# Kernel tuning notes

Measured on AMD Instinct MI355X. Metric: run time of the kernel, lower is better.

The kernel has to match this reference:

```python
import jax, jax.numpy as jnp
import numpy as np

EPS = 1e-5
NB, NP, NA, NROT = 16, 1024, 12, 60
C0, C1 = 64, 128
CIN, CFEAT, COUT = 256, 512, 256


def _bn(x, g, b):
    # training-mode BatchNorm1d: stats over batch (+ spatial) dims, channel dim 1
    axes = (0,) if x.ndim == 2 else (0, 2)
    m = x.mean(axis=axes, keepdims=True)
    v = x.var(axis=axes, keepdims=True)
    sh = [1] * x.ndim; sh[1] = -1
    return (x - m) * jax.lax.rsqrt(v + EPS) * g.reshape(sh) + b.reshape(sh)


def _hat(v):  # (n,3) -> (n,3,3) skew-symmetric
    z = jnp.zeros_like(v[:, 0])
    return jnp.stack([z, -v[:, 2], v[:, 1],
                      v[:, 2], z, -v[:, 0],
                      -v[:, 1], v[:, 0], z], axis=-1).reshape(-1, 3, 3)


def _exp_so3(v):  # Rodrigues formula, (n,3) -> (n,3,3)
    theta = jnp.linalg.norm(v, axis=-1, keepdims=True)  # (n,1)
    k = v / jnp.where(theta < 1e-8, 1.0, theta)
    K = _hat(k)
    s = jnp.sin(theta)[..., None]
    c = (1.0 - jnp.cos(theta))[..., None]
    I = jnp.eye(3, dtype=v.dtype)
    return I + s * K + c * (K @ K)


def _pointnet(xyz, feats, W, b, g, bb):
    # PointnetSO3Conv: concat xyz (expanded over anchors) with feats, 1x1 conv, max over points
    nb, _, npts, na = feats.shape
    x = jnp.concatenate([jnp.broadcast_to(xyz[:, :, :, None], (nb, 3, npts, na)), feats], axis=1)
    y = jnp.einsum('oc,bcpa->bopa', W, x) + b[None, :, None, None]
    y = y.max(axis=2)  # max over points -> (nb, o, na)
    return jax.nn.relu(_bn(y, g, bb))


def setup_inputs() -> dict:
    key = jax.random.key(0)
    ks = iter(jax.random.split(key, 64))
    def nrm(shape, s=0.1):
        return jax.random.normal(next(ks), shape, dtype=jnp.float32) * s
    d = {
        'xyz0': nrm((NB, 3, NP), 1.0),
        'feats0': nrm((NB, C0, NP, NA), 1.0),
        'xyz1': nrm((NB, 3, NP), 1.0),
        'feats1': nrm((NB, C1, NP, NA), 1.0),
        'trace_idx': jax.random.randint(next(ks), (NA, NROT), 0, NA),
        'anchors': nrm((NROT, 3, 3), 1.0),
        'pn0_W': nrm((C0, C0 + 3)), 'pn0_b': nrm((C0,)), 'pn0_g': jnp.ones((C0,), jnp.float32), 'pn0_bb': jnp.zeros((C0,), jnp.float32),
        'pn1_W': nrm((C1, C1 + 3)), 'pn1_b': nrm((C1,)), 'pn1_g': jnp.ones((C1,), jnp.float32), 'pn1_bb': jnp.zeros((C1,), jnp.float32),
        'lin_W': nrm((CIN, C0 + C1)), 'lin_b': nrm((CIN,)), 'lin_g': jnp.ones((CIN,), jnp.float32), 'lin_bb': jnp.zeros((CIN,), jnp.float32),
        'feat_W': nrm((CFEAT, CIN * NA)), 'feat_b': nrm((CFEAT,)), 'feat_g': jnp.ones((CFEAT,), jnp.float32), 'feat_bb': jnp.zeros((CFEAT,), jnp.float32),
        'att_W1': nrm((128, CFEAT)), 'att_b1': nrm((128,)), 'att_g': jnp.ones((128,), jnp.float32), 'att_bb': jnp.zeros((128,), jnp.float32),
        'att_W2': nrm((1, 128)), 'att_b2': nrm((1,)),
        'reg_W1': nrm((128, CFEAT)), 'reg_b1': nrm((128,)), 'reg_g': jnp.ones((128,), jnp.float32), 'reg_bb': jnp.zeros((128,), jnp.float32),
        'reg_W2': nrm((7, 128)), 'reg_b2': nrm((7,)),
        'out_W1': nrm((CFEAT, CFEAT)), 'out_b1': nrm((CFEAT,)), 'out_g': jnp.ones((CFEAT,), jnp.float32), 'out_bb': jnp.zeros((CFEAT,), jnp.float32),
        'out_W2': nrm((COUT, CFEAT)), 'out_b2': nrm((COUT,)),
    }
    return d


def reference(xyz0, feats0, xyz1, feats1, trace_idx, anchors,
              pn0_W, pn0_b, pn0_g, pn0_bb, pn1_W, pn1_b, pn1_g, pn1_bb,
              lin_W, lin_b, lin_g, lin_bb, feat_W, feat_b, feat_g, feat_bb,
              att_W1, att_b1, att_g, att_bb, att_W2, att_b2,
              reg_W1, reg_b1, reg_g, reg_bb, reg_W2, reg_b2,
              out_W1, out_b1, out_g, out_bb, out_W2, out_b2):
    nb = feats0.shape[0]
    # _pooling: per-level pointnet + BN + relu, concat, pn_linear + pn_bn
    p0 = _pointnet(xyz0, feats0, pn0_W, pn0_b, pn0_g, pn0_bb)
    p1 = _pointnet(xyz1, feats1, pn1_W, pn1_b, pn1_g, pn1_bb)
    x = jnp.concatenate([p0, p1], axis=1)                                   # (nb, 192, na)
    x = _bn(jnp.einsum('oc,bca->boa', lin_W, x) + lin_b[None, :, None], lin_g, lin_bb)  # (nb,256,na)
    # gather trace_idx_ori and flatten channel x anchor dims
    x = x[:, :, trace_idx].reshape(nb, CIN * NA, NROT)                      # (nb,3072,60)
    xf = jax.nn.relu(_bn(jnp.einsum('oc,bca->boa', feat_W, x) + feat_b[None, :, None], feat_g, feat_bb))  # (nb,512,60)
    h = jax.nn.relu(_bn(jnp.einsum('oc,bca->boa', reg_W1, xf) + reg_b1[None, :, None], reg_g, reg_bb))
    residual = (jnp.einsum('oc,bca->boa', reg_W2, h) + reg_b2[None, :, None]).transpose(0, 2, 1)  # (nb,60,7)
    res_D = residual[:, :, :3] / jnp.linalg.norm(residual[:, :, :3], axis=-1, keepdims=True)
    res_N = (jax.nn.sigmoid(residual[:, :, 3]) - 0.5) * jnp.pi / 5
    res_V = res_D * res_N[..., None]
    res_R = _exp_so3(res_V.reshape(-1, 3)).reshape(nb, NROT, 3, 3)
    res_T = residual[:, :, 4:]
    pred_R = jnp.einsum('tij,btjk->btik', anchors, res_R)
    # attention head + softmax over 60 rotations
    a = jax.nn.relu(_bn(jnp.einsum('oc,bca->boa', att_W1, xf) + att_b1[None, :, None], att_g, att_bb))
    logits = (jnp.einsum('oc,bca->boa', att_W2, a) + att_b2[None, :, None])[:, 0]   # (nb,60)
    x_attn = jax.nn.softmax(logits, axis=-1)
    # max-pool over rotations + out MLP
    xm = xf.max(axis=-1)                                                    # (nb,512)
    o = jax.nn.relu(_bn(xm @ out_W1.T + out_b1, out_g, out_bb))
    x_out = o @ out_W2.T + out_b2
    return (x_out, x_attn, pred_R, res_T)
```

## Files before the change

kernel.cpp:

```cpp
#include <hip/hip_runtime.h>
#include <math.h>

#define NBATCH 16
#define NPTS   1024
#define NANG   12
#define NROTS  60
#define EPSV   1e-5f

#define WB0_OFF   0
#define WB1_OFF   3072
#define PART0_OFF 13312
#define PART1_OFF 799744
#define XF_OFF    13312
#define XM_OFF    504832
#define OACT_OFF  513024
#define XCAT_OFF  2372608
#define XLIN_OFF  2409472
#define XG_OFF    2458624
#define BRP_OFF   2458624
#define HACT_OFF  4424704
#define AACT_OFF  4547584
#define FRAW_OFF  5407744
#define FEATW_OFF 6882304

#define OUT_XOUT 0
#define OUT_ATTN 4096
#define OUT_PRED 5056
#define OUT_REST 13696

typedef short  bf16x8 __attribute__((ext_vector_type(8)));
typedef float  f32x4  __attribute__((ext_vector_type(4)));

__device__ __forceinline__ unsigned short f2bf_rne(float x){
  unsigned int u = __float_as_uint(x);
  u += 0x7FFFu + ((u >> 16) & 1u);
  return (unsigned short)(u >> 16);
}
__device__ __forceinline__ float bf2f(unsigned short h){
  return __uint_as_float(((unsigned int)h) << 16);
}

__device__ __forceinline__ bf16x8 pack8(const float* f){
  union { unsigned int u[4]; bf16x8 v; } r;
  #pragma unroll
  for (int i = 0; i < 4; i++)
    r.u[i] = __builtin_amdgcn_perm(__float_as_uint(f[2*i+1]),
                                   __float_as_uint(f[2*i]), 0x07060302u);
  return r.v;
}

__device__ __forceinline__ void stage16(const unsigned short* g, unsigned short* l){
  __builtin_amdgcn_global_load_lds((const __attribute__((address_space(1))) void*)g,
                                   (__attribute__((address_space(3))) void*)l, 16, 0, 0);
}

template<int NT>
__device__ __forceinline__ void block_stats(float v, float& m, float& var, float* sbuf){
  constexpr int NW = NT / 64;
  float s = v, s2 = v * v;
  #pragma unroll
  for (int off = 32; off; off >>= 1){
    s  += __shfl_xor(s,  off, 64);
    s2 += __shfl_xor(s2, off, 64);
  }
  const int w = threadIdx.x >> 6;
  if ((threadIdx.x & 63) == 0){ sbuf[w] = s; sbuf[NW + w] = s2; }
  __syncthreads();
  float ts = 0.f, ts2 = 0.f;
  #pragma unroll
  for (int i = 0; i < NW; i++){ ts += sbuf[i]; ts2 += sbuf[NW + i]; }
  m = ts / (float)NT;
  var = ts2 / (float)NT - m * m;
}

template<int C>
__device__ __forceinline__ void prep_wb_body(int idx, const float* __restrict__ W,
                                             unsigned short* __restrict__ Wb){
  constexpr int KPAD = C + 32;
  if (idx >= C * KPAD) return;
  const int o = idx / KPAD, k = idx % KPAD;
  float v = 0.f;
  if (k < C)          v = W[(size_t)o * (C + 3) + 3 + k];
  else if (k < C + 3) v = W[(size_t)o * (C + 3) + (k - C)];
  Wb[idx] = f2bf_rne(v);
}

__global__ __launch_bounds__(256) void prep_all(
    const float* __restrict__ W0, const float* __restrict__ W1,
    const float* __restrict__ FW,
    unsigned short* __restrict__ wb0, unsigned short* __restrict__ wb1,
    unsigned short* __restrict__ fw2){
  const int blk = blockIdx.x;
  if (blk < 24){
    prep_wb_body<64>(blk * 256 + threadIdx.x, W0, wb0);
  } else if (blk < 104){
    prep_wb_body<128>((blk - 24) * 256 + threadIdx.x, W1, wb1);
  } else {
    const int idx = (blk - 104) * 256 + threadIdx.x;
    const int o = idx / 3072, k = idx % 3072;
    const float x = FW[idx];
    const unsigned short hi = f2bf_rne(x);
    const unsigned short lo = f2bf_rne(x - bf2f(hi));
    fw2[(size_t)o * 6144 + k] = hi;
    fw2[(size_t)o * 6144 + 3072 + k] = lo;
  }
}

#define SROW 196
template<int C>
__device__ __forceinline__ void pn_body(
    int nchunk, int b,
    const float* __restrict__ xyz, const float* __restrict__ feats,
    const unsigned short* __restrict__ Wb, float* __restrict__ part,
    float* yb ){
  constexpr int KPAD = C + 32;
  constexpr int NFK  = C / 32;
  constexpr int MTH  = C / 32;
  const int tid  = threadIdx.x;
  const int lane = tid & 63, w = tid >> 6;
  const int wo = w >> 2, wn = w & 3;
  const int g = lane >> 4, l16 = lane & 15;
  const int o_off = wo * (C / 2);
  const int nbase = nchunk * 192;

  int nn[3], pp[3];
  #pragma unroll
  for (int t = 0; t < 3; t++){
    nn[t] = wn * 48 + t * 16 + l16;
    pp[t] = (nbase + nn[t]) / 12;
  }

  f32x4 acc[MTH][3];
  #pragma unroll
  for (int m = 0; m < MTH; m++)
    #pragma unroll
    for (int t = 0; t < 3; t++)
      acc[m][t] = (f32x4){0.f, 0.f, 0.f, 0.f};

  const float* fB = feats + (size_t)b * C * (NPTS * NANG) + nbase;

  float fbuf[2][3][8];
  #pragma unroll
  for (int t = 0; t < 3; t++)
    #pragma unroll
    for (int j = 0; j < 8; j++)
      fbuf[0][t][j] = fB[(size_t)(g * 8 + j) * (NPTS * NANG) + nn[t]];

  #pragma unroll
  for (int ks = 0; ks < NFK; ks++){
    const int cur = ks & 1;
    if (ks + 1 < NFK){
      const int kb = (ks + 1) * 32;
      #pragma unroll
      for (int t = 0; t < 3; t++)
        #pragma unroll
        for (int j = 0; j < 8; j++)
          fbuf[cur ^ 1][t][j] = fB[(size_t)(kb + g * 8 + j) * (NPTS * NANG) + nn[t]];
    }
    const int kb = ks * 32;
    bf16x8 Bf[3];
    #pragma unroll
    for (int t = 0; t < 3; t++) Bf[t] = pack8(fbuf[cur][t]);
    #pragma unroll
    for (int m = 0; m < MTH; m++){
      const bf16x8 Af = *(const bf16x8*)(Wb + (size_t)(o_off + m * 16 + l16) * KPAD + kb + g * 8);
      #pragma unroll
      for (int t = 0; t < 3; t++)
        acc[m][t] = __builtin_amdgcn_mfma_f32_16x16x32_bf16(Af, Bf[t], acc[m][t], 0, 0, 0);
    }
  }

  {
    const int kb = C;
    bf16x8 Bf[3];
    #pragma unroll
    for (int t = 0; t < 3; t++){
      float f[8];
      #pragma unroll
      for (int j = 0; j < 8; j++) f[j] = 0.f;
      if (g == 0){
        #pragma unroll
        for (int j = 0; j < 3; j++)
          f[j] = xyz[(size_t)(b * 3 + j) * NPTS + pp[t]];
      }
      Bf[t] = pack8(f);
    }
    #pragma unroll
    for (int m = 0; m < MTH; m++){
      const bf16x8 Af = *(const bf16x8*)(Wb + (size_t)(o_off + m * 16 + l16) * KPAD + kb + g * 8);
      #pragma unroll
      for (int t = 0; t < 3; t++)
        acc[m][t] = __builtin_amdgcn_mfma_f32_16x16x32_bf16(Af, Bf[t], acc[m][t], 0, 0, 0);
    }
  }

  float* myb = yb + wo * (16 * SROW);
  #pragma unroll
  for (int m = 0; m < MTH; m++){
    __syncthreads();
    #pragma unroll
    for (int t = 0; t < 3; t++)
      #pragma unroll
      for (int r = 0; r < 4; r++)
        myb[(g * 4 + r) * SROW + nn[t]] = acc[m][t][r];
    __syncthreads();
    const int lt = tid & 255;
    if (lt < 192){
      const int o_l = lt / 12, a = lt % 12;
      float mx = -3.4e38f;
      #pragma unroll
      for (int pl = 0; pl < 16; pl++)
        mx = fmaxf(mx, myb[o_l * SROW + pl * 12 + a]);
      part[((size_t)(b * 64 + nchunk) * C + o_off + m * 16 + o_l) * 12 + a] = mx;
    }
  }
}

__global__ __launch_bounds__(512, 4) void pn_both(
    const float* __restrict__ xyz0, const float* __restrict__ feats0,
    const unsigned short* __restrict__ wb0, float* __restrict__ part0,
    const float* __restrict__ xyz1, const float* __restrict__ feats1,
    const unsigned short* __restrict__ wb1, float* __restrict__ part1){
  __shared__ float yb[2 * 16 * SROW];
  const int lin   = blockIdx.x + 64 * (blockIdx.y + 16 * blockIdx.z);
  const int which = lin & 1;
  const int rest  = lin >> 1;
  const int nchunk = rest & 63, b = rest >> 6;
  if (which == 0) pn_body<64> (nchunk, b, xyz0, feats0, wb0, part0, yb);
  else            pn_body<128>(nchunk, b, xyz1, feats1, wb1, part1, yb);
}

__global__ void pn_reduce_bn(const float* __restrict__ part0, const float* __restrict__ part1,
    const float* __restrict__ b0, const float* __restrict__ g0, const float* __restrict__ bb0,
    const float* __restrict__ b1, const float* __restrict__ g1, const float* __restrict__ bb1,
    float* __restrict__ xcat){
  const int ch = blockIdx.x, t = threadIdx.x;
  const int b = t / 12, a = t % 12;
  const float* part; const float *bias, *g, *bb; int o, Cl;
  if (ch < 64){ part = part0; bias = b0; g = g0; bb = bb0; o = ch;      Cl = 64;  }
  else        { part = part1; bias = b1; g = g1; bb = bb1; o = ch - 64; Cl = 128; }
  const float* pp = part + ((size_t)(b * 64) * Cl + o) * 12 + a;
  const size_t kstride = (size_t)Cl * 12;
  float v = pp[0];
  for (int k = 1; k < 64; k++) v = fmaxf(v, pp[(size_t)k * kstride]);
  v += bias[o];
  __shared__ float sbuf[8];
  float m, var;
  block_stats<192>(v, m, var, sbuf);
  float xn = (v - m) * rsqrtf(var + EPSV) * g[o] + bb[o];
  xcat[((size_t)b * 192 + ch) * 12 + a] = fmaxf(xn, 0.f);
}

__global__ void lin_bn(const float* __restrict__ xcat, const float* __restrict__ W,
    const float* __restrict__ bias, const float* __restrict__ g, const float* __restrict__ bb,
    float* __restrict__ xlin){
  const int o = blockIdx.x, t = threadIdx.x;
  const int b = t / 12, a = t % 12;
  const float* xr = xcat + (size_t)b * 2304 + a;
  const float* wr = W + (size_t)o * 192;
  float v = bias[o];
  for (int c = 0; c < 192; c++) v = fmaf(wr[c], xr[(size_t)c * 12], v);
  __shared__ float sbuf[8];
  float m, var;
  block_stats<192>(v, m, var, sbuf);
  xlin[((size_t)b * 256 + o) * 12 + a] = (v - m) * rsqrtf(var + EPSV) * g[o] + bb[o];
}

__global__ void prep_xg(const float* __restrict__ xlin, const int* __restrict__ trace,
                        unsigned short* __restrict__ Xg){
  const int n = blockIdx.x;
  const int b = n / 60, r = n % 60;
  unsigned short* row = Xg + (size_t)n * 6144;
  __shared__ int ta[12];
  if (threadIdx.x < 12) ta[threadIdx.x] = trace[threadIdx.x * 60 + r];
  __syncthreads();
  for (int i = threadIdx.x; i < 3072; i += 256){
    const int c = i / 12, a = i % 12;
    const float x = xlin[((size_t)b * 256 + c) * 12 + ta[a]];
    const unsigned short hi = f2bf_rne(x);
    const unsigned short lo = f2bf_rne(x - bf2f(hi));
    row[i] = hi;
    row[3072 + i] = lo;
  }
}

__global__ __launch_bounds__(256) void feat_mfma(
    const unsigned short* __restrict__ Wb2, const unsigned short* __restrict__ Xg,
    float* __restrict__ fraw){
  const int nblk = blockIdx.x, mblk = blockIdx.y, seg = blockIdx.z;
  const int tid = threadIdx.x;
  const int lane = tid & 63, wave = tid >> 6;
  const int g = lane >> 4, l16 = lane & 15;
  const int kA = (seg == 1) ? 3072 : 0;
  const int kB = (seg == 2) ? 3072 : 0;
  const int sw = l16 & 7;
  const int wm = wave >> 1, wn = wave & 1;

  __shared__ unsigned short As[2][64 * 64];
  __shared__ unsigned short Bs[2][64 * 64];

  int rowj[2], colj[2], ldsoff[2];
  #pragma unroll
  for (int j = 0; j < 2; j++){
    const int idx = j * 256 + wave * 64 + lane;
    rowj[j]   = idx >> 3;
    colj[j]   = ((idx & 7) ^ (rowj[j] & 7)) * 8;
    ldsoff[j] = (j * 256 + wave * 64) * 8;
  }
  const unsigned short* Agb = Wb2 + (size_t)mblk * 64 * 6144 + kA;
  const unsigned short* Bgb = Xg  + (size_t)nblk * 64 * 6144 + kB;

  f32x4 acc[2][2];
  #pragma unroll
  for (int i = 0; i < 2; i++)
    #pragma unroll
    for (int j = 0; j < 2; j++)
      acc[i][j] = (f32x4){0.f, 0.f, 0.f, 0.f};

  #pragma unroll
  for (int j = 0; j < 2; j++){
    stage16(Agb + (size_t)rowj[j] * 6144 + colj[j], &As[0][ldsoff[j]]);
    stage16(Bgb + (size_t)rowj[j] * 6144 + colj[j], &Bs[0][ldsoff[j]]);
  }
  __syncthreads();

  for (int kc = 0; kc < 3072; kc += 64){
    const int buf = (kc >> 6) & 1;
    if (kc + 64 < 3072){
      const int kn = kc + 64;
      #pragma unroll
      for (int j = 0; j < 2; j++){
        stage16(Agb + (size_t)rowj[j] * 6144 + kn + colj[j], &As[buf ^ 1][ldsoff[j]]);
        stage16(Bgb + (size_t)rowj[j] * 6144 + kn + colj[j], &Bs[buf ^ 1][ldsoff[j]]);
      }
    }
    #pragma unroll
    for (int kc2 = 0; kc2 < 64; kc2 += 32){
      const int c0 = kc2 >> 3;
      bf16x8 af[2], bfr[2];
      #pragma unroll
      for (int i = 0; i < 2; i++)
        af[i]  = *(const bf16x8*)&As[buf][(wm * 32 + i * 16 + l16) * 64 + ((c0 + g) ^ sw) * 8];
      #pragma unroll
      for (int i = 0; i < 2; i++)
        bfr[i] = *(const bf16x8*)&Bs[buf][(wn * 32 + i * 16 + l16) * 64 + ((c0 + g) ^ sw) * 8];
      #pragma unroll
      for (int i = 0; i < 2; i++)
        #pragma unroll
        for (int j = 0; j < 2; j++)
          acc[i][j] = __builtin_amdgcn_mfma_f32_16x16x32_bf16(af[i], bfr[j], acc[i][j], 0, 0, 0);
    }
    __syncthreads();
  }

  float* base = fraw + (size_t)seg * (512 * 960);
  #pragma unroll
  for (int i = 0; i < 2; i++)
    #pragma unroll
    for (int j = 0; j < 2; j++){
      const int n = nblk * 64 + wn * 32 + j * 16 + l16;
      #pragma unroll
      for (int q = 0; q < 4; q++){
        const int m = mblk * 64 + wm * 32 + i * 16 + g * 4 + q;
        base[(size_t)m * 960 + n] = acc[i][j][q];
      }
    }
}

__global__ void feat_bn(const float* __restrict__ fraw, const float* __restrict__ bias,
    const float* __restrict__ g, const float* __restrict__ bb,
    float* __restrict__ xf, float* __restrict__ xm){
  const int o = blockIdx.x, t = threadIdx.x;
  const int b = t / 60, r = t % 60;
  const size_t SS = (size_t)512 * 960;
  const size_t in = (size_t)o * 960 + t;
  float v = fraw[in] + fraw[SS + in] + fraw[2 * SS + in] + bias[o];
  __shared__ float sbuf[32];
  float m, var;
  block_stats<960>(v, m, var, sbuf);
  const float xn = fmaxf((v - m) * rsqrtf(var + EPSV) * g[o] + bb[o], 0.f);
  xf[((size_t)b * 512 + o) * 60 + r] = xn;
  __shared__ float red[960];
  red[t] = xn;
  __syncthreads();
  if (r == 0){
    float mx = red[t];
    for (int k = 1; k < 60; k++) mx = fmaxf(mx, red[t + k]);
    xm[(size_t)b * 512 + o] = mx;
  }
}

__global__ __launch_bounds__(256) void brgemm_oh1(const float* __restrict__ xf,
    const float* __restrict__ Wr, const float* __restrict__ Wa,
    float* __restrict__ brp,
    const float* __restrict__ xm, const float* __restrict__ oW1,
    const float* __restrict__ ob1, const float* __restrict__ og,
    const float* __restrict__ obb, float* __restrict__ o_act){
  const int z = blockIdx.z;
  if (z == 16){
    const int q = blockIdx.y * 4 + blockIdx.x;
    if (q >= 32) return;
    const int t = threadIdx.x;
    const int b = t & 15, j = t >> 4;
    const int oc = q * 16 + j;
    float acc = ob1[oc];
    const float* wr = oW1 + (size_t)oc * 512;
    const float* xr = xm + (size_t)b * 512;
    for (int c = 0; c < 512; c++) acc = fmaf(wr[c], xr[c], acc);
    float s = acc, s2 = acc * acc;
    #pragma unroll
    for (int off = 8; off; off >>= 1){
      s  += __shfl_xor(s,  off, 16);
      s2 += __shfl_xor(s2, off, 16);
    }
    const float m = s * (1.f / 16.f);
    const float var = s2 * (1.f / 16.f) - m * m;
    o_act[(size_t)b * 512 + oc] = fmaxf((acc - m) * rsqrtf(var + EPSV) * og[oc] + obb[oc], 0.f);
    return;
  }
  const int og_ = blockIdx.x, b = blockIdx.y;
  const int br = z >> 3, ks = z & 7;
  const float* W = br ? Wa : Wr;
  const int lane = threadIdx.x & 63, wave = threadIdx.x >> 6;
  const int obase = og_ * 32 + wave * 8;
  const int rr = lane < 60 ? lane : 0;
  const float* xb = xf + ((size_t)b * 512 + ks * 64) * 60 + rr;
  const float* wr = W + (size_t)obase * 512 + ks * 64;

  float acc[8];
  #pragma unroll
  for (int i = 0; i < 8; i++) acc[i] = 0.f;

  float cur[4], nxt[4];
  #pragma unroll
  for (int j = 0; j < 4; j++) cur[j] = xb[(size_t)j * 60];

  for (int c0 = 0; c0 < 64; c0 += 4){
    #pragma unroll
    for (int j = 0; j < 4; j++){
      int cc = c0 + 4 + j; if (cc > 63) cc = 63;
      nxt[j] = xb[(size_t)cc * 60];
    }
    #pragma unroll
    for (int j = 0; j < 4; j++)
      #pragma unroll
      for (int i = 0; i < 8; i++)
        acc[i] = fmaf(wr[(size_t)i * 512 + c0 + j], cur[j], acc[i]);
    #pragma unroll
    for (int j = 0; j < 4; j++) cur[j] = nxt[j];
  }

  if (lane < 60){
    #pragma unroll
    for (int i = 0; i < 8; i++)
      brp[(((size_t)z * NBATCH + b) * 128 + obase + i) * 60 + lane] = acc[i];
  }
}

__global__ void br_bn(const float* __restrict__ brp,
    const float* __restrict__ biasR, const float* __restrict__ gR, const float* __restrict__ bbR,
    const float* __restrict__ biasA, const float* __restrict__ gA, const float* __restrict__ bbA,
    float* __restrict__ hact, float* __restrict__ aact){
  const int o = blockIdx.x, br = blockIdx.y, t = threadIdx.x;
  const int b = t / 60, r = t % 60;
  const float* bias = br ? biasA : biasR;
  const float* g    = br ? gA    : gR;
  const float* bb   = br ? bbA   : bbR;
  float v = bias[o];
  #pragma unroll
  for (int ks = 0; ks < 8; ks++)
    v += brp[((((size_t)br * 8 + ks) * NBATCH + b) * 128 + o) * 60 + r];
  __shared__ float sbuf[32];
  float m, var;
  block_stats<960>(v, m, var, sbuf);
  float* outp = br ? aact : hact;
  outp[((size_t)b * 128 + o) * 60 + r] =
      fmaxf((v - m) * rsqrtf(var + EPSV) * g[o] + bb[o], 0.f);
}

__global__ void heads(
    const float* __restrict__ h, const float* __restrict__ rW2,
    const float* __restrict__ rb2, const float* __restrict__ anchors,
    const float* __restrict__ a, const float* __restrict__ aW2, const float* __restrict__ ab2,
    const float* __restrict__ o_act, const float* __restrict__ oW2,
    const float* __restrict__ ob2, float* __restrict__ out){
  const int b = blockIdx.x, sel = blockIdx.y, t = threadIdx.x;
  if (sel == 0){
    if (t >= 64) return;
    const int r = t < 60 ? t : 59;
    float res[7];
    #pragma unroll
    for (int j = 0; j < 7; j++) res[j] = rb2[j];
    for (int c = 0; c < 128; c++){
      const float hv = h[((size_t)b * 128 + c) * 60 + r];
      #pragma unroll
      for (int j = 0; j < 7; j++) res[j] = fmaf(rW2[j * 128 + c], hv, res[j]);
    }
    if (t >= 60) return;
    const float n = sqrtf(res[0]*res[0] + res[1]*res[1] + res[2]*res[2]);
    const float invn = 1.f / n;
    const float Nv = (1.f / (1.f + expf(-res[3])) - 0.5f) * 3.14159265358979323846f / 5.f;
    const float v0 = res[0]*invn*Nv, v1 = res[1]*invn*Nv, v2 = res[2]*invn*Nv;
    const float th = sqrtf(v0*v0 + v1*v1 + v2*v2);
    const float invt = th < 1e-8f ? 1.f : 1.f / th;
    const float k0 = v0*invt, k1 = v1*invt, k2 = v2*invt;
    const float s = sinf(th), cc = 1.f - cosf(th);
    const float K[9] = {0.f, -k2, k1,  k2, 0.f, -k0,  -k1, k0, 0.f};
    float K2[9];
    #pragma unroll
    for (int ii = 0; ii < 3; ii++)
      #pragma unroll
      for (int jj = 0; jj < 3; jj++)
        K2[ii*3+jj] = K[ii*3+0]*K[0*3+jj] + K[ii*3+1]*K[1*3+jj] + K[ii*3+2]*K[2*3+jj];
    float R[9];
    #pragma unroll
    for (int ii = 0; ii < 3; ii++)
      #pragma unroll
      for (int jj = 0; jj < 3; jj++)
        R[ii*3+jj] = (ii == jj ? 1.f : 0.f) + s * K[ii*3+jj] + cc * K2[ii*3+jj];
    const float* A = anchors + (size_t)t * 9;
    #pragma unroll
    for (int ii = 0; ii < 3; ii++)
      #pragma unroll
      for (int kk = 0; kk < 3; kk++){
        const float pv = A[ii*3+0]*R[0*3+kk] + A[ii*3+1]*R[1*3+kk] + A[ii*3+2]*R[2*3+kk];
        out[OUT_PRED + ((size_t)b * 60 + t) * 9 + ii * 3 + kk] = pv;
      }
    #pragma unroll
    for (int k = 0; k < 3; k++)
      out[OUT_REST + ((size_t)b * 60 + t) * 3 + k] = res[4 + k];
  } else if (sel == 1){
    if (t >= 64) return;
    const int r = t < 60 ? t : 59;
    float acc = ab2[0];
    for (int c = 0; c < 128; c++)
      acc = fmaf(aW2[c], a[((size_t)b * 128 + c) * 60 + r], acc);
    const float l = t < 60 ? acc : -INFINITY;
    float mx = l;
    #pragma unroll
    for (int off = 32; off; off >>= 1) mx = fmaxf(mx, __shfl_xor(mx, off, 64));
    const float e = t < 60 ? expf(l - mx) : 0.f;
    float ssum = e;
    #pragma unroll
    for (int off = 32; off; off >>= 1) ssum += __shfl_xor(ssum, off, 64);
    if (t < 60) out[OUT_ATTN + (size_t)b * 60 + t] = e / ssum;
  } else {
    const float* wr = oW2 + (size_t)t * 512;
    const float* xr = o_act + (size_t)b * 512;
    float acc = ob2[t];
    for (int c = 0; c < 512; c++) acc = fmaf(wr[c], xr[c], acc);
    out[OUT_XOUT + (size_t)b * 256 + t] = acc;
  }
}

extern "C" void kernel_launch(void* const* d_in, const int* in_sizes, int n_in,
                              void* d_out, int out_size, void* d_ws, size_t ws_size,
                              hipStream_t stream){
  const float* xyz0    = (const float*)d_in[0];
  const float* feats0  = (const float*)d_in[1];
  const float* xyz1    = (const float*)d_in[2];
  const float* feats1  = (const float*)d_in[3];
  const int*   trace   = (const int*)  d_in[4];
  const float* anchors = (const float*)d_in[5];
  const float* pn0_W  = (const float*)d_in[6];
  const float* pn0_b  = (const float*)d_in[7];
  const float* pn0_g  = (const float*)d_in[8];
  const float* pn0_bb = (const float*)d_in[9];
  const float* pn1_W  = (const float*)d_in[10];
  const float* pn1_b  = (const float*)d_in[11];
  const float* pn1_g  = (const float*)d_in[12];
  const float* pn1_bb = (const float*)d_in[13];
  const float* lin_W  = (const float*)d_in[14];
  const float* lin_b  = (const float*)d_in[15];
  const float* lin_g  = (const float*)d_in[16];
  const float* lin_bb = (const float*)d_in[17];
  const float* feat_W  = (const float*)d_in[18];
  const float* feat_b  = (const float*)d_in[19];
  const float* feat_g  = (const float*)d_in[20];
  const float* feat_bb = (const float*)d_in[21];
  const float* att_W1 = (const float*)d_in[22];
  const float* att_b1 = (const float*)d_in[23];
  const float* att_g  = (const float*)d_in[24];
  const float* att_bb = (const float*)d_in[25];
  const float* att_W2 = (const float*)d_in[26];
  const float* att_b2 = (const float*)d_in[27];
  const float* reg_W1 = (const float*)d_in[28];
  const float* reg_b1 = (const float*)d_in[29];
  const float* reg_g  = (const float*)d_in[30];
  const float* reg_bb = (const float*)d_in[31];
  const float* reg_W2 = (const float*)d_in[32];
  const float* reg_b2 = (const float*)d_in[33];
  const float* out_W1 = (const float*)d_in[34];
  const float* out_b1 = (const float*)d_in[35];
  const float* out_g  = (const float*)d_in[36];
  const float* out_bb = (const float*)d_in[37];
  const float* out_W2 = (const float*)d_in[38];
  const float* out_b2 = (const float*)d_in[39];

  float* ws  = (float*)d_ws;
  float* out = (float*)d_out;
  unsigned short* wb0 = (unsigned short*)(ws + WB0_OFF);
  unsigned short* wb1 = (unsigned short*)(ws + WB1_OFF);
  unsigned short* fw  = (unsigned short*)(ws + FEATW_OFF);
  unsigned short* xg  = (unsigned short*)(ws + XG_OFF);

  prep_all<<<6248, 256, 0, stream>>>(pn0_W, pn1_W, feat_W, wb0, wb1, fw);

  pn_both<<<dim3(64, 16, 2), 512, 0, stream>>>(xyz0, feats0, wb0, ws + PART0_OFF,
                                               xyz1, feats1, wb1, ws + PART1_OFF);

  pn_reduce_bn<<<192, 192, 0, stream>>>(ws + PART0_OFF, ws + PART1_OFF,
      pn0_b, pn0_g, pn0_bb, pn1_b, pn1_g, pn1_bb, ws + XCAT_OFF);

  lin_bn<<<256, 192, 0, stream>>>(ws + XCAT_OFF, lin_W, lin_b, lin_g, lin_bb, ws + XLIN_OFF);

  prep_xg<<<960, 256, 0, stream>>>(ws + XLIN_OFF, trace, xg);

  feat_mfma<<<dim3(15, 8, 3), 256, 0, stream>>>(fw, xg, ws + FRAW_OFF);

  feat_bn<<<512, 960, 0, stream>>>(ws + FRAW_OFF, feat_b, feat_g, feat_bb,
                                   ws + XF_OFF, ws + XM_OFF);

  brgemm_oh1<<<dim3(4, 16, 17), 256, 0, stream>>>(ws + XF_OFF, reg_W1, att_W1, ws + BRP_OFF,
      ws + XM_OFF, out_W1, out_b1, out_g, out_bb, ws + OACT_OFF);

  br_bn<<<dim3(128, 2), 960, 0, stream>>>(ws + BRP_OFF,
      reg_b1, reg_g, reg_bb, att_b1, att_g, att_bb,
      ws + HACT_OFF, ws + AACT_OFF);

  heads<<<dim3(16, 3), 256, 0, stream>>>(ws + HACT_OFF, reg_W2, reg_b2, anchors,
      ws + AACT_OFF, att_W2, att_b2, ws + OACT_OFF, out_W2, out_b2, out);
}
```

Baseline: 433.8 us.

## Pre-transpose point features to bf16 k-packed layout before pointnet MFMA

Adds a transpose stage to the prep kernel that converts feats0/feats1 from fp32 channel-major to a bf16 layout in which each point-anchor holds 32 contiguous channels, using an LDS tile. The pointnet kernel then loads each MFMA B fragment as one 16-byte vector instead of eight strided scalar fp32 loads plus packing. The goal is coalesced, vectorised reads in the GEMM. In exchange it adds a full extra pass that reads fp32 features and writes bf16 copies, and it truncates instead of rounding to nearest even.

New measurement: 466.1 us. +7.4%, slower.

```diff
diff --git a/kernel.cpp b/kernel.cpp
--- a/kernel.cpp
+++ b/kernel.cpp
@@ -22,6 +22,8 @@
 #define AACT_OFF  4547584
 #define FRAW_OFF  5407744
 #define FEATW_OFF 6882304
+#define XP0_OFF   8455168
+#define XP1_OFF   14746624
 
 #define OUT_XOUT 0
 #define OUT_ATTN 4096
@@ -73,6 +75,8 @@
   var = ts2 / (float)NT - m * m;
 }
 
+#define TB0 6248
+#define TB1 7784
 template<int C>
 __device__ __forceinline__ void prep_wb_body(int idx, const float* __restrict__ W,
                                              unsigned short* __restrict__ Wb){
@@ -88,14 +92,21 @@
 __global__ __launch_bounds__(256) void prep_all(
     const float* __restrict__ W0, const float* __restrict__ W1,
     const float* __restrict__ FW,
+    const float* __restrict__ feats0, const float* __restrict__ feats1,
     unsigned short* __restrict__ wb0, unsigned short* __restrict__ wb1,
-    unsigned short* __restrict__ fw2){
+    unsigned short* __restrict__ fw2,
+    unsigned short* __restrict__ xp0, unsigned short* __restrict__ xp1){
+  __shared__ unsigned short tr[32][258];
   const int blk = blockIdx.x;
   if (blk < 24){
     prep_wb_body<64>(blk * 256 + threadIdx.x, W0, wb0);
-  } else if (blk < 104){
+    return;
+  }
+  if (blk < 104){
     prep_wb_body<128>((blk - 24) * 256 + threadIdx.x, W1, wb1);
-  } else {
+    return;
+  }
+  if (blk < TB0){
     const int idx = (blk - 104) * 256 + threadIdx.x;
     const int o = idx / 3072, k = idx % 3072;
     const float x = FW[idx];
@@ -103,14 +114,46 @@
     const unsigned short lo = f2bf_rne(x - bf2f(hi));
     fw2[(size_t)o * 6144 + k] = hi;
     fw2[(size_t)o * 6144 + 3072 + k] = lo;
-  }
+    return;
+  }
+  const float* src; unsigned short* dst;
+  if (blk < TB1){
+    const int tb = blk - TB0;
+    const int nt = tb % 48, kt = tb / 48;
+    src = feats0 + (size_t)kt * 32 * 12288 + nt * 256;
+    dst = xp0 + ((size_t)kt * 12288 + nt * 256) * 32;
+  } else {
+    const int tb = blk - TB1;
+    const int nt = tb % 48, kt = tb / 48;
+    src = feats1 + (size_t)kt * 32 * 12288 + nt * 256;
+    dst = xp1 + ((size_t)kt * 12288 + nt * 256) * 32;
+  }
+  const int t = threadIdx.x;
+  #pragma unroll
+  for (int q = 0; q < 8; q++){
+    const int idx = q * 256 + t;
+    const int rr = idx >> 6, c4 = (idx & 63) << 2;
+    const float4 v = *(const float4*)(src + (size_t)rr * 12288 + c4);
+    tr[rr][c4 + 0] = (unsigned short)(__float_as_uint(v.x) >> 16);
+    tr[rr][c4 + 1] = (unsigned short)(__float_as_uint(v.y) >> 16);
+    tr[rr][c4 + 2] = (unsigned short)(__float_as_uint(v.z) >> 16);
+    tr[rr][c4 + 3] = (unsigned short)(__float_as_uint(v.w) >> 16);
+  }
+  __syncthreads();
+  union { unsigned short s[32]; bf16x8 v8[4]; } ob;
+  #pragma unroll
+  for (int j = 0; j < 32; j++) ob.s[j] = tr[j][t];
+  unsigned short* dp = dst + (size_t)t * 32;
+  #pragma unroll
+  for (int q = 0; q < 4; q++)
+    *(bf16x8*)(dp + q * 8) = ob.v8[q];
 }
 
 #define SROW 196
 template<int C>
 __device__ __forceinline__ void pn_body(
     int nchunk, int b,
-    const float* __restrict__ xyz, const float* __restrict__ feats,
+    const float* __restrict__ xyz, const unsigned short* __restrict__ Xp,
     const unsigned short* __restrict__ Wb, float* __restrict__ part,
     float* yb ){
   constexpr int KPAD = C + 32;
@@ -137,42 +180,29 @@
     for (int t = 0; t < 3; t++)
       acc[m][t] = (f32x4){0.f, 0.f, 0.f, 0.f};
 
-  const float* fB = feats + (size_t)b * C * (NPTS * NANG) + nbase;
-
-  float fbuf[2][3][8];
-  #pragma unroll
-  for (int t = 0; t < 3; t++)
-    #pragma unroll
-    for (int j = 0; j < 8; j++)
-      fbuf[0][t][j] = fB[(size_t)(g * 8 + j) * (NPTS * NANG) + nn[t]];
+  const unsigned short* xbase = Xp + (size_t)b * NFK * 12288 * 32 + g * 8;
+  bf16x8 Bf[NFK][3];
+  #pragma unroll
+  for (int ks = 0; ks < NFK; ks++)
+    #pragma unroll
+    for (int t = 0; t < 3; t++)
+      Bf[ks][t] = *(const bf16x8*)(xbase + ((size_t)ks * 12288 + nbase + nn[t]) * 32);
 
   #pragma unroll
   for (int ks = 0; ks < NFK; ks++){
-    const int cur = ks & 1;
-    if (ks + 1 < NFK){
-      const int kb = (ks + 1) * 32;
-      #pragma unroll
-      for (int t = 0; t < 3; t++)
-        #pragma unroll
-        for (int j = 0; j < 8; j++)
-          fbuf[cur ^ 1][t][j] = fB[(size_t)(kb + g * 8 + j) * (NPTS * NANG) + nn[t]];
-    }
     const int kb = ks * 32;
-    bf16x8 Bf[3];
-    #pragma unroll
-    for (int t = 0; t < 3; t++) Bf[t] = pack8(fbuf[cur][t]);
     #pragma unroll
     for (int m = 0; m < MTH; m++){
       const bf16x8 Af = *(const bf16x8*)(Wb + (size_t)(o_off + m * 16 + l16) * KPAD + kb + g * 8);
       #pragma unroll
       for (int t = 0; t < 3; t++)
-        acc[m][t] = __builtin_amdgcn_mfma_f32_16x16x32_bf16(Af, Bf[t], acc[m][t], 0, 0, 0);
+        acc[m][t] = __builtin_amdgcn_mfma_f32_16x16x32_bf16(Af, Bf[ks][t], acc[m][t], 0, 0, 0);
     }
   }
 
   {
     const int kb = C;
-    bf16x8 Bf[3];
+    bf16x8 Bf2[3];
     #pragma unroll
     for (int t = 0; t < 3; t++){
       float f[8];
@@ -183,14 +213,14 @@
         for (int j = 0; j < 3; j++)
           f[j] = xyz[(size_t)(b * 3 + j) * NPTS + pp[t]];
       }
-      Bf[t] = pack8(f);
+      Bf2[t] = pack8(f);
     }
     #pragma unroll
     for (int m = 0; m < MTH; m++){
       const bf16x8 Af = *(const bf16x8*)(Wb + (size_t)(o_off + m * 16 + l16) * KPAD + kb + g * 8);
       #pragma unroll
       for (int t = 0; t < 3; t++)
-        acc[m][t] = __builtin_amdgcn_mfma_f32_16x16x32_bf16(Af, Bf[t], acc[m][t], 0, 0, 0);
+        acc[m][t] = __builtin_amdgcn_mfma_f32_16x16x32_bf16(Af, Bf2[t], acc[m][t], 0, 0, 0);
     }
   }
 
@@ -217,17 +247,17 @@
 }
 
 __global__ __launch_bounds__(512, 4) void pn_both(
-    const float* __restrict__ xyz0, const float* __restrict__ feats0,
+    const float* __restrict__ xyz0, const unsigned short* __restrict__ xp0,
     const unsigned short* __restrict__ wb0, float* __restrict__ part0,
-    const float* __restrict__ xyz1, const float* __restrict__ feats1,
+    const float* __restrict__ xyz1, const unsigned short* __restrict__ xp1,
     const unsigned short* __restrict__ wb1, float* __restrict__ part1){
   __shared__ float yb[2 * 16 * SROW];
   const int lin   = blockIdx.x + 64 * (blockIdx.y + 16 * blockIdx.z);
   const int which = lin & 1;
   const int rest  = lin >> 1;
   const int nchunk = rest & 63, b = rest >> 6;
-  if (which == 0) pn_body<64> (nchunk, b, xyz0, feats0, wb0, part0, yb);
-  else            pn_body<128>(nchunk, b, xyz1, feats1, wb1, part1, yb);
+  if (which == 0) pn_body<64> (nchunk, b, xyz0, xp0, wb0, part0, yb);
+  else            pn_body<128>(nchunk, b, xyz1, xp1, wb1, part1, yb);
 }
 
 __global__ void pn_reduce_bn(const float* __restrict__ part0, const float* __restrict__ part1,
@@ -603,11 +633,14 @@
   unsigned short* wb1 = (unsigned short*)(ws + WB1_OFF);
   unsigned short* fw  = (unsigned short*)(ws + FEATW_OFF);
   unsigned short* xg  = (unsigned short*)(ws + XG_OFF);
-
-  prep_all<<<6248, 256, 0, stream>>>(pn0_W, pn1_W, feat_W, wb0, wb1, fw);
-
-  pn_both<<<dim3(64, 16, 2), 512, 0, stream>>>(xyz0, feats0, wb0, ws + PART0_OFF,
-                                               xyz1, feats1, wb1, ws + PART1_OFF);
+  unsigned short* xp0 = (unsigned short*)(ws + XP0_OFF);
+  unsigned short* xp1 = (unsigned short*)(ws + XP1_OFF);
+
+  prep_all<<<10856, 256, 0, stream>>>(pn0_W, pn1_W, feat_W, feats0, feats1,
+                                      wb0, wb1, fw, xp0, xp1);
+
+  pn_both<<<dim3(64, 16, 2), 512, 0, stream>>>(xyz0, xp0, wb0, ws + PART0_OFF,
+                                               xyz1, xp1, wb1, ws + PART1_OFF);
 
   pn_reduce_bn<<<192, 192, 0, stream>>>(ws + PART0_OFF, ws + PART1_OFF,
       pn0_b, pn0_g, pn0_bb, pn1_b, pn1_g, pn1_bb, ws + XCAT_OFF);
```
